# Optimization experiments

Measured on AMD Instinct MI355X. Metric: run time of the kernel, lower is better.

Reference implementation:

```python
import jax, jax.numpy as jnp
import numpy as np


def _rgcn_layer(x, rel, adj, W, b):
    # x: [B, N, De], rel: [B, R, Dr], adj: [B, R, N, N]
    # Torch loop: for each r, bmm(adj[:, r], cat([x, rel[:, r] broadcast], -1)), then cat over r.
    B, N, De = x.shape
    R, Dr = rel.shape[1], rel.shape[2]
    h = jnp.concatenate(
        [jnp.broadcast_to(x[:, None], (B, R, N, De)),
         jnp.broadcast_to(rel[:, :, None], (B, R, N, Dr))],
        axis=-1)                                   # [B, R, N, De+Dr]
    # supports, with relation axis placed before features to match torch cat order
    s = jnp.einsum('brmn,brnd->bmrd', adj, h)      # [B, N, R, De+Dr]
    s = s.reshape(B, N, R * (De + Dr))             # [B, N, R*(De+Dr)]
    return s @ W.T + b                             # [B, N, out_dim]


def setup_inputs() -> dict:
    key = jax.random.key(0)
    ks = jax.random.split(key, 6)
    B, N, R = 16, 1024, 10
    De, Dr, H = 64, 32, 64
    cat_in = (De + Dr) * R  # 960
    node_features = jax.random.normal(ks[0], (B, N, De), dtype=jnp.float32)
    relation_features = jax.random.normal(ks[1], (B, R, Dr), dtype=jnp.float32)
    adj = jax.random.uniform(ks[2], (B, R, N, N), dtype=jnp.float32)
    scale0 = np.sqrt(6.0 / (cat_in + H)).astype(np.float32)  # xavier_uniform
    W0 = jax.random.uniform(ks[3], (H, cat_in), minval=-scale0, maxval=scale0, dtype=jnp.float32)
    b0 = jnp.zeros((H,), dtype=jnp.float32)
    W1 = jax.random.uniform(ks[4], (H, cat_in), minval=-scale0, maxval=scale0, dtype=jnp.float32)
    b1 = jnp.zeros((H,), dtype=jnp.float32)
    return {"node_features": node_features, "relation_features": relation_features,
            "adj": adj, "W0": W0, "b0": b0, "W1": W1, "b1": b1}


def reference(node_features, relation_features, adj, W0, b0, W1, b1):
    # StackedRelationalGraphConvolution.forward, 2 layers, no highway,
    # real_valued_graph=False (ReLU), dropout_rate=0 (inference no-op).
    x = jax.nn.relu(_rgcn_layer(node_features, relation_features, adj, W0, b0))
    x = jax.nn.relu(_rgcn_layer(x, relation_features, adj, W1, b1))
    return x
```

## Files before the change

### kernel.cpp

```cpp
#include <hip/hip_runtime.h>
#include <hip/hip_bf16.h>


typedef __bf16 bf16x8 __attribute__((ext_vector_type(8)));
typedef float  f32x4  __attribute__((ext_vector_type(4)));

__global__ __launch_bounds__(256)
void rgcn_prep(const float* __restrict__ x, const float* __restrict__ rel,
               const float* __restrict__ W, __bf16* __restrict__ yt) {
    const int r = blockIdx.y, b = blockIdx.z;
    const int br = b * 10 + r;

    __shared__ float csh[64];
    if (threadIdx.x < 64) {
        const int h = threadIdx.x;
        const float* rp = rel + (size_t)br * 32;
        const float* wp = W + (size_t)h * 960 + r * 96 + 64;
        float a = 0.f;
#pragma unroll
        for (int d = 0; d < 32; ++d) a += rp[d] * wp[d];
        csh[h] = a;
    }
    __syncthreads();

    const int n = blockIdx.x * 256 + threadIdx.x;
    float xr[64];
    const float* xp = x + ((size_t)b * 1024 + n) * 64;
#pragma unroll
    for (int j = 0; j < 16; ++j) {
        const float4 v = *(const float4*)(xp + j * 4);
        xr[j * 4 + 0] = v.x; xr[j * 4 + 1] = v.y;
        xr[j * 4 + 2] = v.z; xr[j * 4 + 3] = v.w;
    }

    const float* wbase = W + r * 96;
    __bf16* yb = yt + ((size_t)br << 16) + n;
    for (int h = 0; h < 64; ++h) {
        float acc = csh[h];
        const float* wr = wbase + (size_t)h * 960;
#pragma unroll
        for (int d = 0; d < 64; ++d) acc += xr[d] * wr[d];
        yb[(size_t)h << 10] = (__bf16)acc;
    }
}

__global__ __launch_bounds__(512, 2)
void rgcn_main(const float* __restrict__ adj, const __bf16* __restrict__ yt,
               const float* __restrict__ bias, float* __restrict__ dst) {
    const int b  = blockIdx.x;
    const int ms = blockIdx.y;
    const int tid = threadIdx.x;
    const int w = tid >> 6, lane = tid & 63;
    const int g = lane >> 4, lm = lane & 15;
    const int l31 = lane & 31, lh = lane >> 5;

    __shared__ __attribute__((aligned(16))) char smem[32768];
    float* shR = (float*)smem;

    const int arow = 2 * w + lh;

    f32x4 ar[8];
    bf16x8 yf[16];
    f32x4 acc[4] = {};

    const float* aptr = adj + (((size_t)(b * 10) * 1024 + ms * 16 + arow) << 10) + l31 * 8;
    const __bf16* ybase = yt + ((size_t)(b * 10) << 16) + ((size_t)lm << 10) + w * 128 + g * 8;

#define ISSUE_A(rr) { const float* ap = aptr + (size_t)(rr) * 1048576;          \
    _Pragma("unroll") for (int i = 0; i < 4; ++i) {                             \
        ar[2*i]   = __builtin_nontemporal_load((const f32x4*)(ap + i * 256));   \
        ar[2*i+1] = __builtin_nontemporal_load((const f32x4*)(ap + i * 256 + 4)); } }

#define LOAD_Y(rr) { const __bf16* yp = ybase + ((size_t)(rr) << 16);           \
    _Pragma("unroll") for (int kc = 0; kc < 4; ++kc)                            \
    _Pragma("unroll") for (int hf = 0; hf < 4; ++hf)                            \
        yf[kc*4+hf] = *(const bf16x8*)(yp + hf * 16384 + kc * 32); }

#define WRITE_A() { _Pragma("unroll") for (int i = 0; i < 4; ++i) {             \
        bf16x8 t8;                                                              \
        _Pragma("unroll") for (int e = 0; e < 4; ++e) {                         \
            t8[e] = (__bf16)ar[2*i][e]; t8[4+e] = (__bf16)ar[2*i+1][e]; }       \
        *(bf16x8*)(smem + arow * 2048 + (((l31 + 32*i) ^ (arow & 7)) << 4)) = t8; } }

#define COMPUTE() { _Pragma("unroll") for (int kc = 0; kc < 4; ++kc) {          \
        const bf16x8 av = *(const bf16x8*)(smem + lm * 2048 +                   \
                            (((w * 16 + kc * 4 + g) ^ (lm & 7)) << 4));         \
        _Pragma("unroll") for (int hf = 0; hf < 4; ++hf)                        \
            acc[hf] = __builtin_amdgcn_mfma_f32_16x16x32_bf16(av, yf[kc*4+hf], acc[hf], 0, 0, 0); } }

    ISSUE_A(0)
    LOAD_Y(0)
    WRITE_A()
    asm volatile("s_waitcnt lgkmcnt(0)" ::: "memory");
    __builtin_amdgcn_sched_barrier(0);
    __builtin_amdgcn_s_barrier();
    __builtin_amdgcn_sched_barrier(0);

    for (int r = 0; r < 10; ++r) {
        if (r < 9) ISSUE_A(r + 1)
        __builtin_amdgcn_sched_barrier(0);
        COMPUTE()
        if (r < 9) LOAD_Y(r + 1)
        __builtin_amdgcn_sched_barrier(0);
        __builtin_amdgcn_s_barrier();
        __builtin_amdgcn_sched_barrier(0);
        if (r < 9) {
            WRITE_A()
            asm volatile("s_waitcnt lgkmcnt(0)" ::: "memory");
        }
        __builtin_amdgcn_sched_barrier(0);
        __builtin_amdgcn_s_barrier();
        __builtin_amdgcn_sched_barrier(0);
    }

#pragma unroll
    for (int hf = 0; hf < 4; ++hf)
#pragma unroll
        for (int reg = 0; reg < 4; ++reg)
            shR[w * 1024 + (g * 4 + reg) * 64 + hf * 16 + lm] = acc[hf][reg];
    asm volatile("s_waitcnt lgkmcnt(0)" ::: "memory");
    __builtin_amdgcn_sched_barrier(0);
    __builtin_amdgcn_s_barrier();
    __builtin_amdgcn_sched_barrier(0);

    {
        const int e0 = tid * 2;
        float s0 = 0.f, s1 = 0.f;
#pragma unroll
        for (int s = 0; s < 8; ++s) {
            s0 += shR[s * 1024 + e0];
            s1 += shR[s * 1024 + e0 + 1];
        }
        const int h0 = e0 & 63;
        s0 = fmaxf(s0 + bias[h0], 0.f);
        s1 = fmaxf(s1 + bias[h0 + 1], 0.f);
        float2 o = {s0, s1};
        *(float2*)(dst + (((size_t)b << 10) + ms * 16) * 64 + e0) = o;
    }
#undef ISSUE_A
#undef LOAD_Y
#undef WRITE_A
#undef COMPUTE
}

extern "C" void kernel_launch(void* const* d_in, const int* in_sizes, int n_in,
                              void* d_out, int out_size, void* d_ws, size_t ws_size,
                              hipStream_t stream) {
    const float* x   = (const float*)d_in[0];
    const float* rel = (const float*)d_in[1];
    const float* adj = (const float*)d_in[2];
    const float* W0  = (const float*)d_in[3];
    const float* b0  = (const float*)d_in[4];
    const float* W1  = (const float*)d_in[5];
    const float* b1  = (const float*)d_in[6];
    float* out = (float*)d_out;

    char* ws = (char*)d_ws;
    __bf16* Yt = (__bf16*)ws;
    float* x2  = (float*)(ws + 20971520);

    for (int layer = 0; layer < 2; ++layer) {
        const float* xin  = layer ? x2 : x;
        const float* W    = layer ? W1 : W0;
        const float* bias = layer ? b1 : b0;
        float* dst        = layer ? out : x2;

        rgcn_prep<<<dim3(4, 10, 16), 256, 0, stream>>>(xin, rel, W, Yt);
        rgcn_main<<<dim3(16, 64), 512, 0, stream>>>(adj, Yt, bias, dst);
    }
}
```

Measured before the change: 646.8 us.

## Load adjacency fragments directly into MFMA registers, drop LDS staging and barriers

Each lane now reads the adjacency elements it needs as the MFMA A operand straight from global memory and converts them to bf16 in registers. This replaces the cooperative load, swizzled LDS write and LDS read, and removes the two block barriers per relation step. Y-fragment prefetch for the next relation is interleaved per output quarter between the MFMAs. The cost is less coalesced adjacency loads (32-byte chunks per lane across 16 rows) and more register pressure from split prefetch buffers.

```diff
diff --git a/kernel.cpp b/kernel.cpp
--- a/kernel.cpp
+++ b/kernel.cpp
@@ -52,76 +52,60 @@
     const int tid = threadIdx.x;
     const int w = tid >> 6, lane = tid & 63;
     const int g = lane >> 4, lm = lane & 15;
-    const int l31 = lane & 31, lh = lane >> 5;
 
-    __shared__ __attribute__((aligned(16))) char smem[32768];
-    float* shR = (float*)smem;
+    const float* abase = adj + (((size_t)(b * 10) * 1024 + ms * 16 + lm) << 10)
+                       + w * 128 + g * 8;
+    const __bf16* ybase = yt + ((size_t)(b * 10) << 16) + ((size_t)lm << 10)
+                        + w * 128 + g * 8;
 
-    const int arow = 2 * w + lh;
-
-    f32x4 ar[8];
-    bf16x8 yf[16];
+    f32x4 pf[8];
+    bf16x8 yq[4][4];
     f32x4 acc[4] = {};
 
-    const float* aptr = adj + (((size_t)(b * 10) * 1024 + ms * 16 + arow) << 10) + l31 * 8;
-    const __bf16* ybase = yt + ((size_t)(b * 10) << 16) + ((size_t)lm << 10) + w * 128 + g * 8;
+#define ISSUE_A(rr) { const float* ap = abase + (size_t)(rr) * 1048576;          \
+    _Pragma("unroll") for (int kc = 0; kc < 4; ++kc) {                           \
+        pf[2*kc]   = __builtin_nontemporal_load((const f32x4*)(ap + kc * 32));   \
+        pf[2*kc+1] = __builtin_nontemporal_load((const f32x4*)(ap + kc * 32 + 4)); } }
 
-#define ISSUE_A(rr) { const float* ap = aptr + (size_t)(rr) * 1048576;          \
-    _Pragma("unroll") for (int i = 0; i < 4; ++i) {                             \
-        ar[2*i]   = __builtin_nontemporal_load((const f32x4*)(ap + i * 256));   \
-        ar[2*i+1] = __builtin_nontemporal_load((const f32x4*)(ap + i * 256 + 4)); } }
-
-#define LOAD_Y(rr) { const __bf16* yp = ybase + ((size_t)(rr) << 16);           \
-    _Pragma("unroll") for (int kc = 0; kc < 4; ++kc)                            \
-    _Pragma("unroll") for (int hf = 0; hf < 4; ++hf)                            \
-        yf[kc*4+hf] = *(const bf16x8*)(yp + hf * 16384 + kc * 32); }
-
-#define WRITE_A() { _Pragma("unroll") for (int i = 0; i < 4; ++i) {             \
-        bf16x8 t8;                                                              \
-        _Pragma("unroll") for (int e = 0; e < 4; ++e) {                         \
-            t8[e] = (__bf16)ar[2*i][e]; t8[4+e] = (__bf16)ar[2*i+1][e]; }       \
-        *(bf16x8*)(smem + arow * 2048 + (((l31 + 32*i) ^ (arow & 7)) << 4)) = t8; } }
-
-#define COMPUTE() { _Pragma("unroll") for (int kc = 0; kc < 4; ++kc) {          \
-        const bf16x8 av = *(const bf16x8*)(smem + lm * 2048 +                   \
-                            (((w * 16 + kc * 4 + g) ^ (lm & 7)) << 4));         \
-        _Pragma("unroll") for (int hf = 0; hf < 4; ++hf)                        \
-            acc[hf] = __builtin_amdgcn_mfma_f32_16x16x32_bf16(av, yf[kc*4+hf], acc[hf], 0, 0, 0); } }
+#define ISSUE_YQ(hf_, rr) { const __bf16* yp = ybase + (((size_t)(rr)) << 16)    \
+                             + (size_t)(hf_) * 16384;                            \
+    _Pragma("unroll") for (int kc = 0; kc < 4; ++kc)                             \
+        yq[hf_][kc] = *(const bf16x8*)(yp + kc * 32); }
 
     ISSUE_A(0)
-    LOAD_Y(0)
-    WRITE_A()
-    asm volatile("s_waitcnt lgkmcnt(0)" ::: "memory");
-    __builtin_amdgcn_sched_barrier(0);
-    __builtin_amdgcn_s_barrier();
-    __builtin_amdgcn_sched_barrier(0);
+#pragma unroll
+    for (int hf = 0; hf < 4; ++hf) ISSUE_YQ(hf, 0)
 
     for (int r = 0; r < 10; ++r) {
+        bf16x8 av[4];
+#pragma unroll
+        for (int kc = 0; kc < 4; ++kc)
+#pragma unroll
+            for (int e = 0; e < 4; ++e) {
+                av[kc][e]     = (__bf16)pf[2*kc][e];
+                av[kc][4 + e] = (__bf16)pf[2*kc+1][e];
+            }
         if (r < 9) ISSUE_A(r + 1)
-        __builtin_amdgcn_sched_barrier(0);
-        COMPUTE()
-        if (r < 9) LOAD_Y(r + 1)
-        __builtin_amdgcn_sched_barrier(0);
-        __builtin_amdgcn_s_barrier();
-        __builtin_amdgcn_sched_barrier(0);
-        if (r < 9) {
-            WRITE_A()
-            asm volatile("s_waitcnt lgkmcnt(0)" ::: "memory");
+
+#pragma unroll
+        for (int hf = 0; hf < 4; ++hf) {
+#pragma unroll
+            for (int kc = 0; kc < 4; ++kc)
+                acc[hf] = __builtin_amdgcn_mfma_f32_16x16x32_bf16(
+                              av[kc], yq[hf][kc], acc[hf], 0, 0, 0);
+            if (r < 9) ISSUE_YQ(hf, r + 1)
         }
-        __builtin_amdgcn_sched_barrier(0);
-        __builtin_amdgcn_s_barrier();
-        __builtin_amdgcn_sched_barrier(0);
     }
+#undef ISSUE_A
+#undef ISSUE_YQ
 
+    __shared__ float shR[8 * 1024];
 #pragma unroll
     for (int hf = 0; hf < 4; ++hf)
 #pragma unroll
         for (int reg = 0; reg < 4; ++reg)
             shR[w * 1024 + (g * 4 + reg) * 64 + hf * 16 + lm] = acc[hf][reg];
-    asm volatile("s_waitcnt lgkmcnt(0)" ::: "memory");
-    __builtin_amdgcn_sched_barrier(0);
-    __builtin_amdgcn_s_barrier();
-    __builtin_amdgcn_sched_barrier(0);
+    __syncthreads();
 
     {
         const int e0 = tid * 2;
@@ -137,10 +121,6 @@
         float2 o = {s0, s1};
         *(float2*)(dst + (((size_t)b << 10) + ms * 16) * 64 + e0) = o;
     }
-#undef ISSUE_A
-#undef LOAD_Y
-#undef WRITE_A
-#undef COMPUTE
 }
 
 extern "C" void kernel_launch(void* const* d_in, const int* in_sizes, int n_in,
```

New measurement: 729.3 us. 12.8% more time.
